# Performance work log

Hardware: AMD Instinct MI355X
Metric: run time of the kernel (lower is better)

The kernel has to match this reference:

```python
import jax, jax.numpy as jnp
import numpy as np

B, S, E, H = 2, 2048, 4096, 32
D = E // H  # head_dim = 128
MAX_SEQ = 2048


def precompute_freqs(dim, end, theta=10000.0):
    # Faithful to the torch source, including its operator precedence:
    # freqs = 1.0 / (theta ** arange(0, dim, 2)[:dim//2].float() / dim)
    # i.e. 1.0 / ((theta ** exps) / dim); overflows to inf in fp32 -> freq 0.
    exps = jnp.arange(0, dim, 2, dtype=jnp.float32)[: dim // 2]
    freqs = 1.0 / (jnp.power(jnp.float32(theta), exps) / jnp.float32(dim))
    t = jnp.arange(end, dtype=jnp.float32)
    f = jnp.outer(t, freqs)  # [end, dim//2]
    return jnp.cos(f), jnp.sin(f)


def apply_rope(x, cos, sin, pos):
    # x: [B,H,S,D]; cos/sin: [max_seq, dim//2]; pos: [B,S]
    c = cos[pos][:, None]  # [B,1,S,f]
    s = sin[pos][:, None]
    xr = x.reshape(*x.shape[:-1], -1, 2)  # [B,H,S,D/2,2]
    x1, x2 = xr[..., 0], xr[..., 1]
    if x1.shape[-1] > c.shape[-1]:
        rep = x1.shape[-1] // c.shape[-1]  # repeat_interleave factor
        c = jnp.repeat(c, rep, axis=-1)
        s = jnp.repeat(s, rep, axis=-1)
    out = jnp.stack([x1 * c - x2 * s, x1 * s + x2 * c], axis=-1)
    return out.reshape(x.shape)


def setup_inputs() -> dict:
    key = jax.random.key(0)
    kx, kq, kk, kv, ko = jax.random.split(key, 5)
    x = jax.random.normal(kx, (B, S, E), jnp.float32)
    scale = 0.02
    Wq = jax.random.normal(kq, (E, E), jnp.float32) * scale
    Wk = jax.random.normal(kk, (E, E), jnp.float32) * scale
    Wv = jax.random.normal(kv, (E, E), jnp.float32) * scale
    Wo = jax.random.normal(ko, (E, E), jnp.float32) * scale
    z = jnp.zeros((E,), jnp.float32)
    return {"x": x, "Wq": Wq, "bq": z, "Wk": Wk, "bk": z, "Wv": Wv, "bv": z, "Wo": Wo, "bo": z}


def reference(x, Wq, bq, Wk, bk, Wv, bv, Wo, bo):
    cos, sin = precompute_freqs(H, MAX_SEQ)  # note: dim = n_heads, as in source
    pos = jnp.broadcast_to(jnp.arange(S)[None, :], (B, S))  # no offset, S <= max
    # QKV projections (torch Linear: x @ W.T + b)
    q = (x @ Wq.T + bq).reshape(B, S, H, D).transpose(0, 2, 1, 3)  # [B,H,S,D]
    k = (x @ Wk.T + bk).reshape(B, S, H, D).transpose(0, 2, 1, 3)
    v = (x @ Wv.T + bv).reshape(B, S, H, D).transpose(0, 2, 1, 3)
    q = apply_rope(q, cos, sin, pos)
    k = apply_rope(k, cos, sin, pos)
    # SDPA with mask=None (non-causal, full attention)
    scores = jnp.einsum("bhqd,bhkd->bhqk", q, k) / np.float32(np.sqrt(D))
    att = jax.nn.softmax(scores, axis=-1)
    out = jnp.einsum("bhqk,bhkd->bhqd", att, v)
    out = out.transpose(0, 2, 1, 3).reshape(B, S, E)
    return out @ Wo.T + bo
```

## Files before the change

### kernel.cpp

```cpp
#include <hip/hip_runtime.h>
#include <math.h>

typedef _Float16 half8 __attribute__((ext_vector_type(8)));
typedef _Float16 half4 __attribute__((ext_vector_type(4)));
typedef __fp16 fp16x2 __attribute__((ext_vector_type(2)));
typedef float f32x4 __attribute__((ext_vector_type(4)));
typedef unsigned uint4v __attribute__((ext_vector_type(4)));

struct FreqT { float f[16]; };

__device__ __forceinline__ f32x4 mfma16(half8 a, half8 b, f32x4 c) {
  return __builtin_amdgcn_mfma_f32_16x16x32_f16(a, b, c, 0, 0, 0);
}

__device__ __forceinline__ void gload_lds16(const void* g, void* l) {
  __builtin_amdgcn_global_load_lds(
      (const __attribute__((address_space(1))) void*)g,
      (__attribute__((address_space(3))) void*)l, 16, 0, 0);
}

__device__ __forceinline__ unsigned pk_f16(float p0, float p1) {
  fp16x2 h = __builtin_amdgcn_cvt_pkrtz(p0, p1);
  return __builtin_bit_cast(unsigned, h);
}

#define S_BARRIER() __builtin_amdgcn_s_barrier()
#define WAIT_LGKM0() asm volatile("s_waitcnt lgkmcnt(0)" ::: "memory")
#define WAIT_VM8() asm volatile("s_waitcnt vmcnt(8)" ::: "memory")
#define WAIT_VM4() asm volatile("s_waitcnt vmcnt(4)" ::: "memory")
#define WAIT_VM0() asm volatile("s_waitcnt vmcnt(0)" ::: "memory")

__global__ __launch_bounds__(256)
void cast_f32_f16(const float* __restrict__ in, _Float16* __restrict__ out, long n8) {
  long i = (long)blockIdx.x * blockDim.x + threadIdx.x;
  if (i >= n8) return;
  float4 a = ((const float4*)in)[2 * i];
  float4 b = ((const float4*)in)[2 * i + 1];
  half8 v;
  v[0] = (_Float16)a.x; v[1] = (_Float16)a.y; v[2] = (_Float16)a.z; v[3] = (_Float16)a.w;
  v[4] = (_Float16)b.x; v[5] = (_Float16)b.y; v[6] = (_Float16)b.z; v[7] = (_Float16)b.w;
  ((half8*)out)[i] = v;
}

#define GBM 256
#define GBN 256
#define GBK 64

template <typename OutT>
__global__ __launch_bounds__(512, 2)
void gemm256(const _Float16* __restrict__ A, const _Float16* __restrict__ W,
             const float* __restrict__ bias, OutT* __restrict__ C,
             int M, int N, int K) {
  __shared__ __align__(16) _Float16 lds[4][GBM * GBK];

  int nwg = gridDim.x;
  int bid = blockIdx.x;
  int cpx = nwg >> 3;
  int swz = (bid & 7) * cpx + (bid >> 3);
  int ntn = N / GBN;
  int m0 = (swz / ntn) * GBM, n0 = (swz % ntn) * GBN;

  int tid = threadIdx.x, lane = tid & 63, w = tid >> 6;
  int wm = w >> 2, wn = w & 3;
  int g = lane >> 4, lc = lane & 15;

  int r8 = w * 8 + (lane >> 3);
  int cs = (((lane & 7) ^ (lane >> 3)) << 3);
  const _Float16* gA = A + (size_t)(m0 + r8) * K + cs;
  const _Float16* gB = W + (size_t)(n0 + r8) * K + cs;

#define STAGE(bi, k0) do {                                            \
    _Float16* la_ = &lds[(bi) * 2][0] + w * 512;                      \
    _Float16* lb_ = &lds[(bi) * 2 + 1][0] + w * 512;                  \
    _Pragma("unroll")                                                 \
    for (int i_ = 0; i_ < 4; ++i_) {                                  \
      gload_lds16(gA + (size_t)(i_ * 64) * K + (k0), la_ + i_ * 4096);\
      gload_lds16(gB + (size_t)(i_ * 64) * K + (k0), lb_ + i_ * 4096);\
    } } while (0)

  int aOff[8], bOff[4];
#pragma unroll
  for (int mf = 0; mf < 8; ++mf) aOff[mf] = (wm * 128 + mf * 16 + lc) * 64;
#pragma unroll
  for (int nf = 0; nf < 4; ++nf) bOff[nf] = (wn * 64 + nf * 16 + lc) * 64;
  int co0 = (((0 * 4 + g) ^ (lc & 7)) << 3);
  int co1 = (((1 * 4 + g) ^ (lc & 7)) << 3);

  half8 a0[8], a1[8], b0[4], b1[4];
  f32x4 acc[8][4] = {};

#define LOAD_SET0(bi) do {                                            \
    const _Float16* lA_ = &lds[(bi) * 2][0];                          \
    const _Float16* lB_ = &lds[(bi) * 2 + 1][0];                      \
    _Pragma("unroll")                                                 \
    for (int mf = 0; mf < 4; ++mf) {                                  \
      a0[mf * 2 + 0] = *(const half8*)&lA_[aOff[mf] + co0];           \
      a0[mf * 2 + 1] = *(const half8*)&lA_[aOff[mf] + co1];           \
    }                                                                 \
    _Pragma("unroll")                                                 \
    for (int nf = 0; nf < 2; ++nf) {                                  \
      b0[nf * 2 + 0] = *(const half8*)&lB_[bOff[nf] + co0];           \
      b0[nf * 2 + 1] = *(const half8*)&lB_[bOff[nf] + co1];           \
    } } while (0)

#define LOAD_SET1(bi) do {                                            \
    const _Float16* lA_ = &lds[(bi) * 2][0];                          \
    const _Float16* lB_ = &lds[(bi) * 2 + 1][0];                      \
    _Pragma("unroll")                                                 \
    for (int mf = 0; mf < 4; ++mf) {                                  \
      a1[mf * 2 + 0] = *(const half8*)&lA_[aOff[mf + 4] + co0];       \
      a1[mf * 2 + 1] = *(const half8*)&lA_[aOff[mf + 4] + co1];       \
    }                                                                 \
    _Pragma("unroll")                                                 \
    for (int nf = 0; nf < 2; ++nf) {                                  \
      b1[nf * 2 + 0] = *(const half8*)&lB_[bOff[nf + 2] + co0];       \
      b1[nf * 2 + 1] = *(const half8*)&lB_[bOff[nf + 2] + co1];       \
    } } while (0)

#define MFMA_Q(mq, nq, ar, br) do {                                   \
    __builtin_amdgcn_s_setprio(1);                                    \
    _Pragma("unroll")                                                 \
    for (int mf = 0; mf < 4; ++mf)                                    \
      _Pragma("unroll")                                               \
      for (int nf = 0; nf < 2; ++nf)                                  \
        _Pragma("unroll")                                             \
        for (int kk = 0; kk < 2; ++kk)                                \
          acc[(mq) * 4 + mf][(nq) * 2 + nf] =                         \
              mfma16(ar[mf * 2 + kk], br[nf * 2 + kk],                \
                     acc[(mq) * 4 + mf][(nq) * 2 + nf]);              \
    __builtin_amdgcn_s_setprio(0); } while (0)

  const int NT = K >> 6;

  STAGE(0, 0);
  STAGE(1, GBK);
  WAIT_VM8();
  S_BARRIER();
  LOAD_SET0(0);

  for (int t = 0; t < NT - 2; ++t) {
    int cur = t & 1;
    LOAD_SET1(cur);
    MFMA_Q(0, 0, a0, b0);
    MFMA_Q(0, 1, a0, b1);
    WAIT_LGKM0();
    S_BARRIER();
    STAGE(cur, (t + 2) << 6);
    MFMA_Q(1, 1, a1, b1);
    MFMA_Q(1, 0, a1, b0);
    WAIT_VM8();
    S_BARRIER();
    LOAD_SET0(cur ^ 1);
  }
  {
    int cur = (NT - 2) & 1;
    LOAD_SET1(cur);
    MFMA_Q(0, 0, a0, b0);
    MFMA_Q(0, 1, a0, b1);
    MFMA_Q(1, 1, a1, b1);
    MFMA_Q(1, 0, a1, b0);
    WAIT_VM0();
    S_BARRIER();
    LOAD_SET0(cur ^ 1);
  }
  {
    LOAD_SET1((NT - 1) & 1);
    MFMA_Q(0, 0, a0, b0);
    MFMA_Q(0, 1, a0, b1);
    MFMA_Q(1, 1, a1, b1);
    MFMA_Q(1, 0, a1, b0);
  }

  int crow = m0 + wm * 128 + g * 4;
  int ccol = n0 + wn * 64 + lc;
#pragma unroll
  for (int nf = 0; nf < 4; ++nf) {
    float bv = bias[ccol + nf * 16];
#pragma unroll
    for (int mf = 0; mf < 8; ++mf)
#pragma unroll
      for (int j = 0; j < 4; ++j)
        C[(size_t)(crow + mf * 16 + j) * N + ccol + nf * 16] =
            (OutT)(acc[mf][nf][j] + bv);
  }
#undef STAGE
#undef LOAD_SET0
#undef LOAD_SET1
#undef MFMA_Q
}

__global__ __launch_bounds__(256)
void rope_kernel(_Float16* __restrict__ x, FreqT ft, int Sn, int E, long n8) {
  long i = (long)blockIdx.x * blockDim.x + threadIdx.x;
  if (i >= n8) return;
  int epr = E / 8;
  int e8 = (int)(i % epr);
  int s = (int)((i / epr) % Sn);
  int fj = e8 & 15;
  float fr = ft.f[fj];
  float ang = (float)s * fr;
  float sv, cv;
  sincosf(ang, &sv, &cv);
  half8 v = ((const half8*)x)[i];
  half8 o;
#pragma unroll
  for (int p = 0; p < 4; ++p) {
    float x1 = (float)v[2 * p], x2 = (float)v[2 * p + 1];
    o[2 * p] = (_Float16)(x1 * cv - x2 * sv);
    o[2 * p + 1] = (_Float16)(x1 * sv + x2 * cv);
  }
  ((half8*)x)[i] = o;
}

__global__ __launch_bounds__(256)
void transpose_v(const _Float16* __restrict__ v, _Float16* __restrict__ vt,
                 int Hn, int Sn) {
  const int D = 128;
  const int E = Hn * D;
  __shared__ _Float16 t[64][130];
  int spb = Sn / 64;
  int bid = blockIdx.x;
  int s0 = (bid % spb) * 64;
  int bh = bid / spb;
  int b = bh / Hn, h = bh % Hn;
  int tid = threadIdx.x;
  int r = tid >> 2, dc = (tid & 3) * 32;
  const _Float16* src = v + (size_t)(b * Sn + s0 + r) * E + h * D + dc;
#pragma unroll
  for (int i = 0; i < 4; ++i) {
    half8 x = *(const half8*)(src + i * 8);
#pragma unroll
    for (int k = 0; k < 4; ++k) {
      _Float16 a0 = x[2 * k], a1 = x[2 * k + 1];
      t[r][dc + i * 8 + 2 * k] = a0;
      t[r][dc + i * 8 + 2 * k + 1] = a1;
    }
  }
  __syncthreads();
  int d = tid >> 1, sh = (tid & 1) * 32;
  half8 ov[4];
#pragma unroll
  for (int c = 0; c < 4; ++c)
#pragma unroll
    for (int j = 0; j < 8; ++j)
      ov[c][j] = t[sh + c * 8 + j][d];
  _Float16* dst = vt + ((size_t)bh * D + d) * Sn + s0 + sh;
#pragma unroll
  for (int c = 0; c < 4; ++c)
    *(half8*)(dst + c * 8) = ov[c];
}

#define QB 128
#define KB 64

__global__ __launch_bounds__(256, 2)
void flash_attn(const _Float16* __restrict__ qg, const _Float16* __restrict__ kg,
                const _Float16* __restrict__ vt, _Float16* __restrict__ og,
                int Bn, int Hn, int Sn) {
  const int D = 128;
  const int E = Hn * D;

  __shared__ _Float16 Ksh[2][KB * 128];
  __shared__ _Float16 Vsh[2][D * KB];
  __shared__ float sm[4][32];

  int qtiles = Sn / QB;
  int nwg = gridDim.x;
  int bid = blockIdx.x;
  int swzb = (bid & 7) * (nwg >> 3) + (bid >> 3);
  int bh = swzb / qtiles, qt = swzb % qtiles;
  int b = bh / Hn, h = bh % Hn;

  int tid = threadIdx.x, lane = tid & 63, w = tid >> 6;
  int g = lane >> 4, lc = lane & 15;
  int lc7 = lc & 7;

  const size_t headoff = ((size_t)b * Sn) * E + (size_t)h * D;
  const _Float16* qp = qg + headoff;
  const _Float16* kp = kg + headoff;
  const _Float16* vtp = vt + (size_t)(b * Hn + h) * D * Sn;

  int q0 = qt * QB + w * 32;
  half8 aq[2][4];
#pragma unroll
  for (int mf = 0; mf < 2; ++mf)
#pragma unroll
    for (int kf = 0; kf < 4; ++kf)
      aq[mf][kf] = *(const half8*)(qp + (size_t)(q0 + mf * 16 + lc) * E + kf * 32 + g * 8);

  float mrun[2] = {-1e30f, -1e30f}, lpart[2] = {0.f, 0.f};
  f32x4 o[2][8] = {};

  const float scale = 0.08838834764831845f;

  int krow = 4 * w + (lane >> 4);
  int kcol = ((lane & 15) ^ (krow & 7)) * 8;
  const _Float16* gK = kp + (size_t)krow * E + kcol;
  int vrow = w * 32 + (lane >> 3);
  int vcol = ((lane & 7) ^ (vrow & 7)) * 8;
  const _Float16* gV = vtp + (size_t)vrow * Sn + vcol;

  float* smw = sm[w];

  const int NT = Sn / KB;

#define STAGE_K(buf, kt) do {                                          \
    _Float16* lK_ = Ksh[buf] + w * 512;                                \
    _Pragma("unroll")                                                  \
    for (int i_ = 0; i_ < 4; ++i_)                                     \
      gload_lds16(gK + (size_t)((kt) * KB + 16 * i_) * E, lK_ + i_ * 2048); \
  } while (0)
#define STAGE_V(buf, kt) do {                                          \
    _Float16* lV_ = Vsh[buf] + w * 2048;                               \
    _Pragma("unroll")                                                  \
    for (int p_ = 0; p_ < 4; ++p_)                                     \
      gload_lds16(gV + (size_t)(p_ * 8) * Sn + (kt) * KB, lV_ + p_ * 512); \
  } while (0)

  STAGE_K(0, 0);
  STAGE_K(1, 1);
  STAGE_V(0, 0);
  WAIT_VM8();
  S_BARRIER();

  for (int t = 0; t < NT; ++t) {
    int c = t & 1;

    f32x4 st[2][4] = {};
    {
      const _Float16* Kc = Ksh[c];
      __builtin_amdgcn_s_setprio(1);
#pragma unroll
      for (int kf = 0; kf < 4; ++kf) {
        half8 bk[4];
#pragma unroll
        for (int nf = 0; nf < 4; ++nf)
          bk[nf] = *(const half8*)&Kc[(nf * 16 + lc) * 128 + (((kf * 4 + g) ^ lc7) << 3)];
#pragma unroll
        for (int nf = 0; nf < 4; ++nf)
#pragma unroll
          for (int mf = 0; mf < 2; ++mf)
            st[mf][nf] = mfma16(bk[nf], aq[mf][kf], st[mf][nf]);
      }
      __builtin_amdgcn_s_setprio(0);
    }
    WAIT_LGKM0();
    S_BARRIER();

    if (t + 1 < NT) STAGE_V(c ^ 1, t + 1);
    if (t + 2 < NT) STAGE_K(c, t + 2);

    bool resc[2];
#pragma unroll
    for (int mf = 0; mf < 2; ++mf) {
      f32x4 m4 = st[mf][0];
#pragma unroll
      for (int nf = 1; nf < 4; ++nf)
#pragma unroll
        for (int j = 0; j < 4; ++j) m4[j] = fmaxf(m4[j], st[mf][nf][j]);
      float mx = fmaxf(fmaxf(m4[0], m4[1]), fmaxf(m4[2], m4[3]));
      mx = fmaxf(mx, __shfl_xor(mx, 16));
      mx = fmaxf(mx, __shfl_xor(mx, 32));
      mx *= scale;
      resc[mf] = __any(mx > mrun[mf] + 8.f);
      if (resc[mf]) {
        float mnew = fmaxf(mrun[mf], mx);
        float r = __expf(mrun[mf] - mnew);
        mrun[mf] = mnew;
        lpart[mf] *= r;
        if (g == 0) smw[mf * 16 + lc] = r;
      }
    }
#pragma unroll
    for (int mf = 0; mf < 2; ++mf)
      if (resc[mf]) {
        f32x4 rv = *(const f32x4*)&smw[mf * 16 + g * 4];
#pragma unroll
        for (int df = 0; df < 8; ++df)
#pragma unroll
          for (int j = 0; j < 4; ++j) o[mf][df][j] *= rv[j];
      }

    half8 pa00, pa01, pa10, pa11;
#define PACK_P(MF, PA0, PA1) do {                                          \
      float e0, e1;                                                        \
      e0 = __expf(st[MF][0][0] * scale - mrun[MF]);                        \
      e1 = __expf(st[MF][0][1] * scale - mrun[MF]);                        \
      lpart[MF] += e0 + e1; unsigned k00 = pk_f16(e0, e1);                 \
      e0 = __expf(st[MF][0][2] * scale - mrun[MF]);                        \
      e1 = __expf(st[MF][0][3] * scale - mrun[MF]);                        \
      lpart[MF] += e0 + e1; unsigned k01 = pk_f16(e0, e1);                 \
      e0 = __expf(st[MF][1][0] * scale - mrun[MF]);                        \
      e1 = __expf(st[MF][1][1] * scale - mrun[MF]);                        \
      lpart[MF] += e0 + e1; unsigned k10 = pk_f16(e0, e1);                 \
      e0 = __expf(st[MF][1][2] * scale - mrun[MF]);                        \
      e1 = __expf(st[MF][1][3] * scale - mrun[MF]);                        \
      lpart[MF] += e0 + e1; unsigned k11 = pk_f16(e0, e1);                 \
      e0 = __expf(st[MF][2][0] * scale - mrun[MF]);                        \
      e1 = __expf(st[MF][2][1] * scale - mrun[MF]);                        \
      lpart[MF] += e0 + e1; unsigned k20 = pk_f16(e0, e1);                 \
      e0 = __expf(st[MF][2][2] * scale - mrun[MF]);                        \
      e1 = __expf(st[MF][2][3] * scale - mrun[MF]);                        \
      lpart[MF] += e0 + e1; unsigned k21 = pk_f16(e0, e1);                 \
      e0 = __expf(st[MF][3][0] * scale - mrun[MF]);                        \
      e1 = __expf(st[MF][3][1] * scale - mrun[MF]);                        \
      lpart[MF] += e0 + e1; unsigned k30 = pk_f16(e0, e1);                 \
      e0 = __expf(st[MF][3][2] * scale - mrun[MF]);                        \
      e1 = __expf(st[MF][3][3] * scale - mrun[MF]);                        \
      lpart[MF] += e0 + e1; unsigned k31 = pk_f16(e0, e1);                 \
      asm("v_permlane32_swap_b32 %0, %1" : "+v"(k00), "+v"(k10));          \
      asm("v_permlane16_swap_b32 %0, %1" : "+v"(k00), "+v"(k10));          \
      asm("v_permlane32_swap_b32 %0, %1" : "+v"(k01), "+v"(k11));          \
      asm("v_permlane16_swap_b32 %0, %1" : "+v"(k01), "+v"(k11));          \
      asm("v_permlane32_swap_b32 %0, %1" : "+v"(k20), "+v"(k30));          \
      asm("v_permlane16_swap_b32 %0, %1" : "+v"(k20), "+v"(k30));          \
      asm("v_permlane32_swap_b32 %0, %1" : "+v"(k21), "+v"(k31));          \
      asm("v_permlane16_swap_b32 %0, %1" : "+v"(k21), "+v"(k31));          \
      uint4v p0v, p1v;                                                     \
      p0v[0] = k00; p0v[1] = k01; p0v[2] = k10; p0v[3] = k11;              \
      p1v[0] = k20; p1v[1] = k21; p1v[2] = k30; p1v[3] = k31;              \
      PA0 = __builtin_bit_cast(half8, p0v);                                \
      PA1 = __builtin_bit_cast(half8, p1v);                                \
    } while (0)
    PACK_P(0, pa00, pa01);
    PACK_P(1, pa10, pa11);
#undef PACK_P

    if (t + 2 < NT) { WAIT_VM8(); }
    else if (t + 1 < NT) { WAIT_VM4(); }
    else { WAIT_VM0(); }
    S_BARRIER();

    __builtin_amdgcn_s_setprio(1);
    {
      const _Float16* Vc = Vsh[c];
      int csw0 = (g ^ lc7) << 3;
      int csw1 = ((4 + g) ^ lc7) << 3;
#pragma unroll
      for (int df = 0; df < 8; ++df) {
        half8 bv0 = *(const half8*)&Vc[(df * 16 + lc) * 64 + csw0];
        o[0][df] = mfma16(pa00, bv0, o[0][df]);
        o[1][df] = mfma16(pa10, bv0, o[1][df]);
      }
#pragma unroll
      for (int df = 0; df < 8; ++df) {
        half8 bv1 = *(const half8*)&Vc[(df * 16 + lc) * 64 + csw1];
        o[0][df] = mfma16(pa01, bv1, o[0][df]);
        o[1][df] = mfma16(pa11, bv1, o[1][df]);
      }
    }
    __builtin_amdgcn_s_setprio(0);
  }
#undef STAGE_K
#undef STAGE_V

#pragma unroll
  for (int mf = 0; mf < 2; ++mf) {
    float l = lpart[mf];
    l += __shfl_xor(l, 16);
    l += __shfl_xor(l, 32);
    if (g == 0) smw[mf * 16 + lc] = 1.0f / l;
  }
  _Float16* op = og + headoff;
#pragma unroll
  for (int mf = 0; mf < 2; ++mf) {
    f32x4 li = *(const f32x4*)&smw[mf * 16 + g * 4];
#pragma unroll
    for (int j = 0; j < 4; ++j) {
      int row = q0 + mf * 16 + g * 4 + j;
#pragma unroll
      for (int df = 0; df < 8; ++df)
        op[(size_t)row * E + df * 16 + lc] = (_Float16)(o[mf][df][j] * li[j]);
    }
  }
}

extern "C" void kernel_launch(void* const* d_in, const int* in_sizes, int n_in,
                              void* d_out, int out_size, void* d_ws, size_t ws_size,
                              hipStream_t stream) {
  const float* x  = (const float*)d_in[0];
  const float* Wq = (const float*)d_in[1];
  const float* bq = (const float*)d_in[2];
  const float* Wk = (const float*)d_in[3];
  const float* bk = (const float*)d_in[4];
  const float* Wv = (const float*)d_in[5];
  const float* bv = (const float*)d_in[6];
  const float* Wo = (const float*)d_in[7];
  const float* bo = (const float*)d_in[8];

  const int E = in_sizes[2];
  const int M = in_sizes[0] / E;
  const int S = 2048;
  const int Bb = M / S;
  const int H = 32;

  _Float16* xh = (_Float16*)d_ws;
  _Float16* wh = xh + (size_t)M * E;
  _Float16* qh = wh + (size_t)E * E;
  _Float16* kh = qh + (size_t)M * E;
  _Float16* vh = kh + (size_t)M * E;
  _Float16* oh = xh;
  _Float16* vtb = wh;

  FreqT ft;
  for (int j = 0; j < 16; ++j) {
    float pf = (float)pow(10000.0, (double)(2 * j));
    ft.f[j] = 1.0f / (pf / 32.0f);
  }

  long nx8 = (long)M * E / 8;
  long nw8 = (long)E * E / 8;
  dim3 blk(256);
  int cb_x = (int)((nx8 + 255) / 256);
  int cb_w = (int)((nw8 + 255) / 256);
  int gemm_grid = (M / GBM) * (E / GBN);

  cast_f32_f16<<<cb_x, blk, 0, stream>>>(x, xh, nx8);

  cast_f32_f16<<<cb_w, blk, 0, stream>>>(Wq, wh, nw8);
  gemm256<_Float16><<<gemm_grid, 512, 0, stream>>>(xh, wh, bq, qh, M, E, E);
  cast_f32_f16<<<cb_w, blk, 0, stream>>>(Wk, wh, nw8);
  gemm256<_Float16><<<gemm_grid, 512, 0, stream>>>(xh, wh, bk, kh, M, E, E);
  cast_f32_f16<<<cb_w, blk, 0, stream>>>(Wv, wh, nw8);
  gemm256<_Float16><<<gemm_grid, 512, 0, stream>>>(xh, wh, bv, vh, M, E, E);

  rope_kernel<<<cb_x, blk, 0, stream>>>(qh, ft, S, E, nx8);
  rope_kernel<<<cb_x, blk, 0, stream>>>(kh, ft, S, E, nx8);

  transpose_v<<<Bb * H * (S / 64), blk, 0, stream>>>(vh, vtb, H, S);

  flash_attn<<<Bb * H * (S / QB), blk, 0, stream>>>(qh, kh, vtb, oh, Bb, H, S);

  cast_f32_f16<<<cb_w, blk, 0, stream>>>(Wo, wh, nw8);
  gemm256<float><<<gemm_grid, 512, 0, stream>>>(oh, wh, bo, (float*)d_out, M, E, E);
}
```

Baseline: 763.7 us.

## Interleave LDS reads with MFMAs in GEMM and fold softmax scale into Q

The GEMM main loop now splits fragment reads into separate B1 and A1 phases. Partial lgkmcnt waits and extra barriers let LDS reads overlap with MFMA quadrants, where before a full load set completed first. The attention softmax scale and log2(e) are folded into the Q projection epilogue, so flash attention can use raw exp2 without a per-element multiply, and the rescale threshold is adjusted to match. The extra barriers per iteration may add synchronisation cost, and scaling Q in fp16 before RoPE slightly changes rounding.

New measurement: 772.2 us. No clear change (+1.1%).

```diff
diff --git a/kernel.cpp b/kernel.cpp
--- a/kernel.cpp
+++ b/kernel.cpp
@@ -26,6 +26,8 @@
 
 #define S_BARRIER() __builtin_amdgcn_s_barrier()
 #define WAIT_LGKM0() asm volatile("s_waitcnt lgkmcnt(0)" ::: "memory")
+#define WAIT_LGKM4() asm volatile("s_waitcnt lgkmcnt(4)" ::: "memory")
+#define WAIT_LGKM8() asm volatile("s_waitcnt lgkmcnt(8)" ::: "memory")
 #define WAIT_VM8() asm volatile("s_waitcnt vmcnt(8)" ::: "memory")
 #define WAIT_VM4() asm volatile("s_waitcnt vmcnt(4)" ::: "memory")
 #define WAIT_VM0() asm volatile("s_waitcnt vmcnt(0)" ::: "memory")
@@ -50,7 +52,7 @@
 __global__ __launch_bounds__(512, 2)
 void gemm256(const _Float16* __restrict__ A, const _Float16* __restrict__ W,
              const float* __restrict__ bias, OutT* __restrict__ C,
-             int M, int N, int K) {
+             int M, int N, int K, float smul) {
   __shared__ __align__(16) _Float16 lds[4][GBM * GBK];
 
   int nwg = gridDim.x;
@@ -83,13 +85,13 @@
   for (int mf = 0; mf < 8; ++mf) aOff[mf] = (wm * 128 + mf * 16 + lc) * 64;
 #pragma unroll
   for (int nf = 0; nf < 4; ++nf) bOff[nf] = (wn * 64 + nf * 16 + lc) * 64;
-  int co0 = (((0 * 4 + g) ^ (lc & 7)) << 3);
-  int co1 = (((1 * 4 + g) ^ (lc & 7)) << 3);
+  int co0 = ((g ^ (lc & 7)) << 3);
+  int co1 = (((4 + g) ^ (lc & 7)) << 3);
 
   half8 a0[8], a1[8], b0[4], b1[4];
   f32x4 acc[8][4] = {};
 
-#define LOAD_SET0(bi) do {                                            \
+#define READ_A0B0(bi) do {                                            \
     const _Float16* lA_ = &lds[(bi) * 2][0];                          \
     const _Float16* lB_ = &lds[(bi) * 2 + 1][0];                      \
     _Pragma("unroll")                                                 \
@@ -103,18 +105,20 @@
       b0[nf * 2 + 1] = *(const half8*)&lB_[bOff[nf] + co1];           \
     } } while (0)
 
-#define LOAD_SET1(bi) do {                                            \
+#define READ_B1(bi) do {                                              \
+    const _Float16* lB_ = &lds[(bi) * 2 + 1][0];                      \
+    _Pragma("unroll")                                                 \
+    for (int nf = 0; nf < 2; ++nf) {                                  \
+      b1[nf * 2 + 0] = *(const half8*)&lB_[bOff[nf + 2] + co0];       \
+      b1[nf * 2 + 1] = *(const half8*)&lB_[bOff[nf + 2] + co1];       \
+    } } while (0)
+
+#define READ_A1(bi) do {                                              \
     const _Float16* lA_ = &lds[(bi) * 2][0];                          \
-    const _Float16* lB_ = &lds[(bi) * 2 + 1][0];                      \
     _Pragma("unroll")                                                 \
     for (int mf = 0; mf < 4; ++mf) {                                  \
       a1[mf * 2 + 0] = *(const half8*)&lA_[aOff[mf + 4] + co0];       \
       a1[mf * 2 + 1] = *(const half8*)&lA_[aOff[mf + 4] + co1];       \
-    }                                                                 \
-    _Pragma("unroll")                                                 \
-    for (int nf = 0; nf < 2; ++nf) {                                  \
-      b1[nf * 2 + 0] = *(const half8*)&lB_[bOff[nf + 2] + co0];       \
-      b1[nf * 2 + 1] = *(const half8*)&lB_[bOff[nf + 2] + co1];       \
     } } while (0)
 
 #define MFMA_Q(mq, nq, ar, br) do {                                   \
@@ -136,39 +140,53 @@
   STAGE(1, GBK);
   WAIT_VM8();
   S_BARRIER();
-  LOAD_SET0(0);
+  READ_A0B0(0);
 
   for (int t = 0; t < NT - 2; ++t) {
     int cur = t & 1;
-    LOAD_SET1(cur);
+    READ_B1(cur);
+    WAIT_LGKM4();
     MFMA_Q(0, 0, a0, b0);
+    S_BARRIER();
+    READ_A1(cur);
+    WAIT_LGKM8();
     MFMA_Q(0, 1, a0, b1);
+    S_BARRIER();
     WAIT_LGKM0();
+    MFMA_Q(1, 1, a1, b1);
     S_BARRIER();
     STAGE(cur, (t + 2) << 6);
+    MFMA_Q(1, 0, a1, b0);
+    WAIT_VM8();
+    S_BARRIER();
+    READ_A0B0(cur ^ 1);
+  }
+  {
+    int cur = (NT - 2) & 1;
+    READ_B1(cur);
+    WAIT_LGKM4();
+    MFMA_Q(0, 0, a0, b0);
+    S_BARRIER();
+    READ_A1(cur);
+    WAIT_LGKM8();
+    MFMA_Q(0, 1, a0, b1);
+    S_BARRIER();
+    WAIT_LGKM0();
     MFMA_Q(1, 1, a1, b1);
     MFMA_Q(1, 0, a1, b0);
-    WAIT_VM8();
-    S_BARRIER();
-    LOAD_SET0(cur ^ 1);
+    WAIT_VM0();
+    S_BARRIER();
+    READ_A0B0(cur ^ 1);
   }
   {
-    int cur = (NT - 2) & 1;
-    LOAD_SET1(cur);
+    int cur = (NT - 1) & 1;
+    READ_B1(cur);
+    READ_A1(cur);
+    WAIT_LGKM0();
     MFMA_Q(0, 0, a0, b0);
     MFMA_Q(0, 1, a0, b1);
     MFMA_Q(1, 1, a1, b1);
     MFMA_Q(1, 0, a1, b0);
-    WAIT_VM0();
-    S_BARRIER();
-    LOAD_SET0(cur ^ 1);
-  }
-  {
-    LOAD_SET1((NT - 1) & 1);
-    MFMA_Q(0, 0, a0, b0);
-    MFMA_Q(0, 1, a0, b1);
-    MFMA_Q(1, 1, a1, b1);
-    MFMA_Q(1, 0, a1, b0);
   }
 
   int crow = m0 + wm * 128 + g * 4;
@@ -181,11 +199,12 @@
 #pragma unroll
       for (int j = 0; j < 4; ++j)
         C[(size_t)(crow + mf * 16 + j) * N + ccol + nf * 16] =
-            (OutT)(acc[mf][nf][j] + bv);
+            (OutT)((acc[mf][nf][j] + bv) * smul);
   }
 #undef STAGE
-#undef LOAD_SET0
-#undef LOAD_SET1
+#undef READ_A0B0
+#undef READ_B1
+#undef READ_A1
 #undef MFMA_Q
 }
 
@@ -252,6 +271,7 @@
 
 #define QB 128
 #define KB 64
+#define THR2 11.541561f
 
 __global__ __launch_bounds__(256, 2)
 void flash_attn(const _Float16* __restrict__ qg, const _Float16* __restrict__ kg,
@@ -290,8 +310,6 @@
 
   float mrun[2] = {-1e30f, -1e30f}, lpart[2] = {0.f, 0.f};
   f32x4 o[2][8] = {};
-
-  const float scale = 0.08838834764831845f;
 
   int krow = 4 * w + (lane >> 4);
   int kcol = ((lane & 15) ^ (krow & 7)) * 8;
@@ -361,11 +379,10 @@
       float mx = fmaxf(fmaxf(m4[0], m4[1]), fmaxf(m4[2], m4[3]));
       mx = fmaxf(mx, __shfl_xor(mx, 16));
       mx = fmaxf(mx, __shfl_xor(mx, 32));
-      mx *= scale;
-      resc[mf] = __any(mx > mrun[mf] + 8.f);
+      resc[mf] = __any(mx > mrun[mf] + THR2);
       if (resc[mf]) {
         float mnew = fmaxf(mrun[mf], mx);
-        float r = __expf(mrun[mf] - mnew);
+        float r = __builtin_amdgcn_exp2f(mrun[mf] - mnew);
         mrun[mf] = mnew;
         lpart[mf] *= r;
         if (g == 0) smw[mf * 16 + lc] = r;
@@ -384,29 +401,29 @@
     half8 pa00, pa01, pa10, pa11;
 #define PACK_P(MF, PA0, PA1) do {                                          \
       float e0, e1;                                                        \
-      e0 = __expf(st[MF][0][0] * scale - mrun[MF]);                        \
-      e1 = __expf(st[MF][0][1] * scale - mrun[MF]);                        \
+      e0 = __builtin_amdgcn_exp2f(st[MF][0][0] - mrun[MF]);                \
+      e1 = __builtin_amdgcn_exp2f(st[MF][0][1] - mrun[MF]);                \
       lpart[MF] += e0 + e1; unsigned k00 = pk_f16(e0, e1);                 \
-      e0 = __expf(st[MF][0][2] * scale - mrun[MF]);                        \
-      e1 = __expf(st[MF][0][3] * scale - mrun[MF]);                        \
+      e0 = __builtin_amdgcn_exp2f(st[MF][0][2] - mrun[MF]);                \
+      e1 = __builtin_amdgcn_exp2f(st[MF][0][3] - mrun[MF]);                \
       lpart[MF] += e0 + e1; unsigned k01 = pk_f16(e0, e1);                 \
-      e0 = __expf(st[MF][1][0] * scale - mrun[MF]);                        \
-      e1 = __expf(st[MF][1][1] * scale - mrun[MF]);                        \
+      e0 = __builtin_amdgcn_exp2f(st[MF][1][0] - mrun[MF]);                \
+      e1 = __builtin_amdgcn_exp2f(st[MF][1][1] - mrun[MF]);                \
       lpart[MF] += e0 + e1; unsigned k10 = pk_f16(e0, e1);                 \
-      e0 = __expf(st[MF][1][2] * scale - mrun[MF]);                        \
-      e1 = __expf(st[MF][1][3] * scale - mrun[MF]);                        \
+      e0 = __builtin_amdgcn_exp2f(st[MF][1][2] - mrun[MF]);                \
+      e1 = __builtin_amdgcn_exp2f(st[MF][1][3] - mrun[MF]);                \
       lpart[MF] += e0 + e1; unsigned k11 = pk_f16(e0, e1);                 \
-      e0 = __expf(st[MF][2][0] * scale - mrun[MF]);                        \
-      e1 = __expf(st[MF][2][1] * scale - mrun[MF]);                        \
+      e0 = __builtin_amdgcn_exp2f(st[MF][2][0] - mrun[MF]);                \
+      e1 = __builtin_amdgcn_exp2f(st[MF][2][1] - mrun[MF]);                \
       lpart[MF] += e0 + e1; unsigned k20 = pk_f16(e0, e1);                 \
-      e0 = __expf(st[MF][2][2] * scale - mrun[MF]);                        \
-      e1 = __expf(st[MF][2][3] * scale - mrun[MF]);                        \
+      e0 = __builtin_amdgcn_exp2f(st[MF][2][2] - mrun[MF]);                \
+      e1 = __builtin_amdgcn_exp2f(st[MF][2][3] - mrun[MF]);                \
       lpart[MF] += e0 + e1; unsigned k21 = pk_f16(e0, e1);                 \
-      e0 = __expf(st[MF][3][0] * scale - mrun[MF]);                        \
-      e1 = __expf(st[MF][3][1] * scale - mrun[MF]);                        \
+      e0 = __builtin_amdgcn_exp2f(st[MF][3][0] - mrun[MF]);                \
+      e1 = __builtin_amdgcn_exp2f(st[MF][3][1] - mrun[MF]);                \
       lpart[MF] += e0 + e1; unsigned k30 = pk_f16(e0, e1);                 \
-      e0 = __expf(st[MF][3][2] * scale - mrun[MF]);                        \
-      e1 = __expf(st[MF][3][3] * scale - mrun[MF]);                        \
+      e0 = __builtin_amdgcn_exp2f(st[MF][3][2] - mrun[MF]);                \
+      e1 = __builtin_amdgcn_exp2f(st[MF][3][3] - mrun[MF]);                \
       lpart[MF] += e0 + e1; unsigned k31 = pk_f16(e0, e1);                 \
       asm("v_permlane32_swap_b32 %0, %1" : "+v"(k00), "+v"(k10));          \
       asm("v_permlane16_swap_b32 %0, %1" : "+v"(k00), "+v"(k10));          \
@@ -508,6 +525,8 @@
     ft.f[j] = 1.0f / (pf / 32.0f);
   }
 
+  const float qs = 0.08838834764831845f * 1.4426950408889634f;
+
   long nx8 = (long)M * E / 8;
   long nw8 = (long)E * E / 8;
   dim3 blk(256);
@@ -518,11 +537,11 @@
   cast_f32_f16<<<cb_x, blk, 0, stream>>>(x, xh, nx8);
 
   cast_f32_f16<<<cb_w, blk, 0, stream>>>(Wq, wh, nw8);
-  gemm256<_Float16><<<gemm_grid, 512, 0, stream>>>(xh, wh, bq, qh, M, E, E);
+  gemm256<_Float16><<<gemm_grid, 512, 0, stream>>>(xh, wh, bq, qh, M, E, E, qs);
   cast_f32_f16<<<cb_w, blk, 0, stream>>>(Wk, wh, nw8);
-  gemm256<_Float16><<<gemm_grid, 512, 0, stream>>>(xh, wh, bk, kh, M, E, E);
+  gemm256<_Float16><<<gemm_grid, 512, 0, stream>>>(xh, wh, bk, kh, M, E, E, 1.0f);
   cast_f32_f16<<<cb_w, blk, 0, stream>>>(Wv, wh, nw8);
-  gemm256<_Float16><<<gemm_grid, 512, 0, stream>>>(xh, wh, bv, vh, M, E, E);
+  gemm256<_Float16><<<gemm_grid, 512, 0, stream>>>(xh, wh, bv, vh, M, E, E, 1.0f);
 
   rope_kernel<<<cb_x, blk, 0, stream>>>(qh, ft, S, E, nx8);
   rope_kernel<<<cb_x, blk, 0, stream>>>(kh, ft, S, E, nx8);
@@ -532,5 +551,5 @@
   flash_attn<<<Bb * H * (S / QB), blk, 0, stream>>>(qh, kh, vtb, oh, Bb, H, S);
 
   cast_f32_f16<<<cb_w, blk, 0, stream>>>(Wo, wh, nw8);
-  gemm256<float><<<gemm_grid, 512, 0, stream>>>(oh, wh, bo, (float*)d_out, M, E, E);
-}
+  gemm256<float><<<gemm_grid, 512, 0, stream>>>(oh, wh, bo, (float*)d_out, M, E, E, 1.0f);
+}
```
